# Kernel optimization log

Hardware: AMD Instinct MI355X
Metric: run time of the kernel (lower is better)

## Reference

```python
import jax, jax.numpy as jnp
import numpy as np

V, E, HN, HH, D, T, B = 10000, 512, 1024, 256, 4, 128, 64


def setup_inputs() -> dict:
    key = jax.random.key(0)
    ks = jax.random.split(key, 9)
    s = lambda k, shape: jax.random.normal(k, shape, jnp.float32) * 0.02
    return {
        "x": jax.random.randint(ks[0], (B, T), 0, V),
        "embed": s(ks[1], (V, E)),
        "Whh": s(ks[2], (2 * HH, HH)), "bhh": jnp.zeros((2 * HH,), jnp.float32),
        "Wih": s(ks[3], (2 * HH, E)), "bih": jnp.zeros((2 * HH,), jnp.float32),
        "Wh": s(ks[4], (2 * HN, HN)), "bh": jnp.zeros((2 * HN,), jnp.float32),
        "Wi": s(ks[5], (2 * HN, E)), "bi": jnp.zeros((2 * HN,), jnp.float32),
        "Wup": s(ks[6], (HN, HH)), "bup": jnp.zeros((HN,), jnp.float32),
        "Wout": s(ks[7], (V, HN)), "bout": jnp.zeros((V,), jnp.float32),
    }


def _gate(Ws, s):
    # highwayGate: split into carry/transform halves (eval mode: no gate dropout)
    hh, tt = jnp.split(Ws, 2, axis=1)
    tt = jax.nn.sigmoid(tt)
    return jnp.tanh(hh) * tt + s * (1.0 - tt)


def reference(x, embed, Whh, bhh, Wih, bih, Wh, bh, Wi, bi, Wup, bup, Wout, bout):
    emb = embed[x]                      # [B, T, E]
    xs = jnp.swapaxes(emb, 0, 1)        # [T, B, E] for scan over time

    def step(carry, xt):
        sH, sN = carry
        for i in range(D):  # depth: weights SHARED across all i (ModuleList(depth*[m]))
            Ws = sH @ Whh.T + bhh
            if i == 0:
                Ws = Ws + xt @ Wih.T + bih
            sH = _gate(Ws, sH)
            z = sH @ Wup.T + bup        # [B, HN]
            zz = jnp.concatenate([z, z], axis=1)  # scale both gate halves
            Ws = (sN @ Wh.T + bh) * zz  # HyperLinear: row-scaled linear
            if i == 0:
                Ws = Ws + (xt @ Wi.T + bi) * zz
            sN = _gate(Ws, sN)
        return (sH, sN), sN

    init = (jnp.zeros((B, HH), jnp.float32), jnp.zeros((B, HN), jnp.float32))
    _, outs = jax.lax.scan(step, init, xs)   # outs: [T, B, HN]
    h = jnp.swapaxes(outs, 0, 1)             # [B, T, HN]
    return h @ Wout.T + bout                 # [B, T, V]
```

## Files before the change

### kernel.cpp

```cpp
#include <hip/hip_runtime.h>
#include <hip/hip_cooperative_groups.h>

namespace cg = cooperative_groups;

typedef float v2f __attribute__((ext_vector_type(2)));

#define B_  64
#define T_  128
#define E_  512
#define HH_ 256
#define HN_ 1024
#define D_  4
#define V_  10000
#define NR_ (T_*D_)
#define NWG_ 256

#define WH_STR   1032
#define WI_STR   520
#define WS_STR   264
#define WH_OFF   0
#define WU_OFF   8256
#define WI_OFF   9312
#define WHH_OFF  13472
#define WIH_OFF  21920
#define LDS_FLOATS 38560

__device__ __forceinline__ float row16_sum(float x) {
    int v = __builtin_bit_cast(int, x);
    x += __builtin_bit_cast(float, __builtin_amdgcn_update_dpp(0, v, 0xB1, 0xF, 0xF, true));
    v = __builtin_bit_cast(int, x);
    x += __builtin_bit_cast(float, __builtin_amdgcn_update_dpp(0, v, 0x4E, 0xF, 0xF, true));
    v = __builtin_bit_cast(int, x);
    x += __builtin_bit_cast(float, __builtin_amdgcn_update_dpp(0, v, 0x124, 0xF, 0xF, true));
    v = __builtin_bit_cast(int, x);
    x += __builtin_bit_cast(float, __builtin_amdgcn_update_dpp(0, v, 0x128, 0xF, 0xF, true));
    return x;
}

__device__ __forceinline__ float sel4(int s, float a, float b, float c, float d) {
    return s == 0 ? a : (s == 1 ? b : (s == 2 ? c : d));
}

__device__ __forceinline__ void flag_barrier(int* __restrict__ flags,
                                             int* __restrict__ gen,
                                             int w, int tau, int target)
{
    __syncthreads();
    if (tau == 0) {
        __builtin_amdgcn_fence(__ATOMIC_RELEASE, "agent");
        __hip_atomic_store(&flags[w * 16], target, __ATOMIC_RELAXED,
                           __HIP_MEMORY_SCOPE_AGENT);
    }
    if (w == 0) {
        if (tau < NWG_) {
            while (__hip_atomic_load(&flags[tau * 16], __ATOMIC_RELAXED,
                                     __HIP_MEMORY_SCOPE_AGENT) < target) {
                __builtin_amdgcn_s_sleep(1);
            }
        }
        __syncthreads();
        if (tau == 0)
            __hip_atomic_store(gen, target, __ATOMIC_RELAXED,
                               __HIP_MEMORY_SCOPE_AGENT);
    } else if (tau == 0) {
        while (__hip_atomic_load(gen, __ATOMIC_RELAXED,
                                 __HIP_MEMORY_SCOPE_AGENT) < target) {
            __builtin_amdgcn_s_sleep(1);
        }
    }
    if (tau == 0)
        __builtin_amdgcn_fence(__ATOMIC_ACQUIRE, "agent");
    __syncthreads();
}

__global__ __launch_bounds__(1024, 1) void recur_kernel(
    const int*   __restrict__ xx,
    const float* __restrict__ embed,
    const float* __restrict__ Whh, const float* __restrict__ bhh,
    const float* __restrict__ Wih, const float* __restrict__ bih,
    const float* __restrict__ Wh,  const float* __restrict__ bh,
    const float* __restrict__ Wi,  const float* __restrict__ bi,
    const float* __restrict__ Wup, const float* __restrict__ bup,
    float* __restrict__ sH,
    float* __restrict__ sN,
    float* __restrict__ hOut,
    int*   __restrict__ flags,
    int*   __restrict__ gen)
{
    extern __shared__ float lds[];
    cg::grid_group grid = cg::this_grid();
    const int w   = blockIdx.x;
    const int tau = threadIdx.x;
    const int gid = w * 1024 + tau;
    const int ch0 = (w & 15) * 16;

    for (int idx = tau; idx < 2048; idx += 1024) {
        int r = idx >> 8, kq = idx & 255;
        int grow = w*4 + (r & 3) + (r >> 2) * HN_;
        *(float4*)&lds[WH_OFF + r*WH_STR + kq*4] =
            *(const float4*)(Wh + (size_t)grow * HN_ + kq*4);
    }
    if (tau < 256) {
        int r = tau >> 6, kq = tau & 63;
        *(float4*)&lds[WU_OFF + r*WS_STR + kq*4] =
            *(const float4*)(Wup + (size_t)(w*4 + r) * HH_ + kq*4);
    }
    if (tau < 1024) {
        int r = tau >> 7, kq = tau & 127;
        int grow = w*4 + (r & 3) + (r >> 2) * HN_;
        *(float4*)&lds[WI_OFF + r*WI_STR + kq*4] =
            *(const float4*)(Wi + (size_t)grow * E_ + kq*4);
    }
    for (int idx = tau; idx < 2048; idx += 1024) {
        int r = idx >> 6, kq = idx & 63;
        int grow = ch0 + (r & 15) + (r >> 4) * HH_;
        *(float4*)&lds[WHH_OFF + r*WS_STR + kq*4] =
            *(const float4*)(Whh + (size_t)grow * HH_ + kq*4);
    }
    for (int idx = tau; idx < 4096; idx += 1024) {
        int r = idx >> 7, kq = idx & 127;
        int grow = ch0 + (r & 15) + (r >> 4) * HH_;
        *(float4*)&lds[WIH_OFF + r*WI_STR + kq*4] =
            *(const float4*)(Wih + (size_t)grow * E_ + kq*4);
    }

    if (gid < B_ * HH_) sH[gid] = 0.f;
    if (gid < B_ * HN_) sN[B_ * HN_ + gid] = 0.f;
    if (tau == 0) flags[w * 16] = 0;
    if (w == 0 && tau == 0) *gen = 0;
    __syncthreads();
    grid.sync();

    const int lane = tau & 63;
    const int bq   = tau >> 6;
    const int kk   = lane & 15;
    const int jj   = lane >> 4;

    const int j = w * 4 + jj;
    const float bh1 = bh[j],  bh2 = bh[j + HN_];
    const float bi1 = bi[j],  bi2 = bi[j + HN_];
    const float bupj = bup[j];
    const float* wrow1 = lds + WH_OFF + jj * WH_STR;
    const float* wrow2 = lds + WH_OFF + (4 + jj) * WH_STR;
    const float* urow  = lds + WU_OFF + jj * WS_STR;
    const float* yrow1 = lds + WI_OFF + jj * WI_STR;
    const float* yrow2 = lds + WI_OFF + (4 + jj) * WI_STR;

    const int ch = ch0 + bq;
    const int bH = (w >> 4) * 4 + jj;
    const float bhh1 = bhh[ch], bhh2 = bhh[ch + HH_];
    const float bih1 = bih[ch], bih2 = bih[ch + HH_];
    const float* qrow1 = lds + WHH_OFF + bq * WS_STR;
    const float* qrow2 = lds + WHH_OFF + (16 + bq) * WS_STR;
    const float* prow1 = lds + WIH_OFF + bq * WI_STR;
    const float* prow2 = lds + WIH_OFF + (16 + bq) * WI_STR;

    for (int r = 0; r <= NR_; ++r) {
        const int p = r & 1;
        const float* sNp = sN + p * (B_ * HN_);
        const float* sHp = sH + p * (B_ * HH_);
        float* sNn = sN + (1 - p) * (B_ * HN_);
        float* sHn = sH + (1 - p) * (B_ * HH_);

        if (r >= 1) {
            const int s = r - 1;
            const int t = s >> 2;
            const int i = s & 3;

            const float* sb0 = sNp + (bq * 4 + 0) * HN_;
            const float* sb1 = sNp + (bq * 4 + 1) * HN_;
            const float* sb2 = sNp + (bq * 4 + 2) * HN_;
            const float* sb3 = sNp + (bq * 4 + 3) * HN_;

            v2f A1[4], A2[4], Z[4];
            #pragma unroll
            for (int bb = 0; bb < 4; ++bb) { A1[bb] = (v2f){0.f,0.f}; A2[bb] = (v2f){0.f,0.f}; Z[bb] = (v2f){0.f,0.f}; }

            #pragma unroll
            for (int u = 0; u < 16; ++u) {
                const int fi = (u * 16 + kk) * 4;
                float4 w1 = *(const float4*)(wrow1 + fi);
                float4 w2 = *(const float4*)(wrow2 + fi);
                float4 s0 = *(const float4*)(sb0 + fi);
                float4 s1 = *(const float4*)(sb1 + fi);
                float4 s2 = *(const float4*)(sb2 + fi);
                float4 s3 = *(const float4*)(sb3 + fi);
                v2f w1l = {w1.x, w1.y}, w1h = {w1.z, w1.w};
                v2f w2l = {w2.x, w2.y}, w2h = {w2.z, w2.w};
                v2f a;
                a = (v2f){s0.x, s0.y}; A1[0] += a * w1l; A2[0] += a * w2l;
                a = (v2f){s0.z, s0.w}; A1[0] += a * w1h; A2[0] += a * w2h;
                a = (v2f){s1.x, s1.y}; A1[1] += a * w1l; A2[1] += a * w2l;
                a = (v2f){s1.z, s1.w}; A1[1] += a * w1h; A2[1] += a * w2h;
                a = (v2f){s2.x, s2.y}; A1[2] += a * w1l; A2[2] += a * w2l;
                a = (v2f){s2.z, s2.w}; A1[2] += a * w1h; A2[2] += a * w2h;
                a = (v2f){s3.x, s3.y}; A1[3] += a * w1l; A2[3] += a * w2l;
                a = (v2f){s3.z, s3.w}; A1[3] += a * w1h; A2[3] += a * w2h;
            }

            if (i == 0) {
                const int t0 = xx[(bq * 4 + 0) * T_ + t];
                const int t1 = xx[(bq * 4 + 1) * T_ + t];
                const int t2 = xx[(bq * 4 + 2) * T_ + t];
                const int t3 = xx[(bq * 4 + 3) * T_ + t];
                const float* e0 = embed + (size_t)t0 * E_;
                const float* e1 = embed + (size_t)t1 * E_;
                const float* e2 = embed + (size_t)t2 * E_;
                const float* e3 = embed + (size_t)t3 * E_;
                #pragma unroll
                for (int u = 0; u < 8; ++u) {
                    const int fi = (u * 16 + kk) * 4;
                    float4 y1 = *(const float4*)(yrow1 + fi);
                    float4 y2 = *(const float4*)(yrow2 + fi);
                    float4 v0 = *(const float4*)(e0 + fi);
                    float4 v1 = *(const float4*)(e1 + fi);
                    float4 v2 = *(const float4*)(e2 + fi);
                    float4 v3 = *(const float4*)(e3 + fi);
                    v2f y1l = {y1.x, y1.y}, y1h = {y1.z, y1.w};
                    v2f y2l = {y2.x, y2.y}, y2h = {y2.z, y2.w};
                    v2f a;
                    a = (v2f){v0.x, v0.y}; A1[0] += a * y1l; A2[0] += a * y2l;
                    a = (v2f){v0.z, v0.w}; A1[0] += a * y1h; A2[0] += a * y2h;
                    a = (v2f){v1.x, v1.y}; A1[1] += a * y1l; A2[1] += a * y2l;
                    a = (v2f){v1.z, v1.w}; A1[1] += a * y1h; A2[1] += a * y2h;
                    a = (v2f){v2.x, v2.y}; A1[2] += a * y1l; A2[2] += a * y2l;
                    a = (v2f){v2.z, v2.w}; A1[2] += a * y1h; A2[2] += a * y2h;
                    a = (v2f){v3.x, v3.y}; A1[3] += a * y1l; A2[3] += a * y2l;
                    a = (v2f){v3.z, v3.w}; A1[3] += a * y1h; A2[3] += a * y2h;
                }
            }

            {
                const float* hb0 = sHp + (bq * 4 + 0) * HH_;
                const float* hb1 = sHp + (bq * 4 + 1) * HH_;
                const float* hb2 = sHp + (bq * 4 + 2) * HH_;
                const float* hb3 = sHp + (bq * 4 + 3) * HH_;
                #pragma unroll
                for (int u = 0; u < 4; ++u) {
                    const int fi = (u * 16 + kk) * 4;
                    float4 uw = *(const float4*)(urow + fi);
                    float4 h0 = *(const float4*)(hb0 + fi);
                    float4 h1 = *(const float4*)(hb1 + fi);
                    float4 h2 = *(const float4*)(hb2 + fi);
                    float4 h3 = *(const float4*)(hb3 + fi);
                    v2f ul = {uw.x, uw.y}, uh = {uw.z, uw.w};
                    v2f a;
                    a = (v2f){h0.x, h0.y}; Z[0] += a * ul;
                    a = (v2f){h0.z, h0.w}; Z[0] += a * uh;
                    a = (v2f){h1.x, h1.y}; Z[1] += a * ul;
                    a = (v2f){h1.z, h1.w}; Z[1] += a * uh;
                    a = (v2f){h2.x, h2.y}; Z[2] += a * ul;
                    a = (v2f){h2.z, h2.w}; Z[2] += a * uh;
                    a = (v2f){h3.x, h3.y}; Z[3] += a * ul;
                    a = (v2f){h3.z, h3.w}; Z[3] += a * uh;
                }
            }

            float a1r0 = row16_sum(A1[0].x + A1[0].y);
            float a1r1 = row16_sum(A1[1].x + A1[1].y);
            float a1r2 = row16_sum(A1[2].x + A1[2].y);
            float a1r3 = row16_sum(A1[3].x + A1[3].y);
            float a2r0 = row16_sum(A2[0].x + A2[0].y);
            float a2r1 = row16_sum(A2[1].x + A2[1].y);
            float a2r2 = row16_sum(A2[2].x + A2[2].y);
            float a2r3 = row16_sum(A2[3].x + A2[3].y);
            float zr0  = row16_sum(Z[0].x + Z[0].y);
            float zr1  = row16_sum(Z[1].x + Z[1].y);
            float zr2  = row16_sum(Z[2].x + Z[2].y);
            float zr3  = row16_sum(Z[3].x + Z[3].y);

            const int bsel = bq * 4 + (kk & 3);
            const float ov = sNp[bsel * HN_ + j];

            if (kk < 4) {
                float g1 = sel4(kk, a1r0, a1r1, a1r2, a1r3) + bh1;
                float g2 = sel4(kk, a2r0, a2r1, a2r2, a2r3) + bh2;
                if (i == 0) { g1 += bi1; g2 += bi2; }
                const float zv  = sel4(kk, zr0, zr1, zr2, zr3) + bupj;
                const float g_h = g1 * zv;
                const float g_t = g2 * zv;
                const float sg  = 1.f / (1.f + expf(-g_t));
                const float nv  = tanhf(g_h) * sg + ov * (1.f - sg);
                sNn[bsel * HN_ + j] = nv;
                if (i == D_ - 1) hOut[(size_t)(bsel * T_ + t) * HN_ + j] = nv;
            }
        }

        if (r < NR_) {
            const int t = r >> 2;
            const int i = r & 3;
            v2f a1v = {0.f, 0.f}, a2v = {0.f, 0.f};
            const float* shb = sHp + bH * HH_;
            #pragma unroll
            for (int uu = 0; uu < 4; ++uu) {
                const int fi = (((jj + uu) & 3) * 16 + kk) * 4;
                float4 q1 = *(const float4*)(qrow1 + fi);
                float4 q2 = *(const float4*)(qrow2 + fi);
                float4 sv = *(const float4*)(shb + fi);
                v2f q1l = {q1.x, q1.y}, q1h = {q1.z, q1.w};
                v2f q2l = {q2.x, q2.y}, q2h = {q2.z, q2.w};
                v2f a;
                a = (v2f){sv.x, sv.y}; a1v += a * q1l; a2v += a * q2l;
                a = (v2f){sv.z, sv.w}; a1v += a * q1h; a2v += a * q2h;
            }
            if (i == 0) {
                const int tok = xx[bH * T_ + t];
                const float* eb = embed + (size_t)tok * E_;
                #pragma unroll
                for (int uu = 0; uu < 4; ++uu) {
                    const int fi = (((jj + uu) & 3) * 16 + kk) * 4;
                    float4 p1a = *(const float4*)(prow1 + fi);
                    float4 p1b = *(const float4*)(prow1 + fi + 256);
                    float4 p2a = *(const float4*)(prow2 + fi);
                    float4 p2b = *(const float4*)(prow2 + fi + 256);
                    float4 ea  = *(const float4*)(eb + fi);
                    float4 eb2 = *(const float4*)(eb + fi + 256);
                    v2f a;
                    a = (v2f){ea.x, ea.y};  a1v += a * (v2f){p1a.x, p1a.y}; a2v += a * (v2f){p2a.x, p2a.y};
                    a = (v2f){ea.z, ea.w};  a1v += a * (v2f){p1a.z, p1a.w}; a2v += a * (v2f){p2a.z, p2a.w};
                    a = (v2f){eb2.x, eb2.y}; a1v += a * (v2f){p1b.x, p1b.y}; a2v += a * (v2f){p2b.x, p2b.y};
                    a = (v2f){eb2.z, eb2.w}; a1v += a * (v2f){p1b.z, p1b.w}; a2v += a * (v2f){p2b.z, p2b.w};
                }
            }
            float a1 = row16_sum(a1v.x + a1v.y);
            float a2 = row16_sum(a2v.x + a2v.y);
            const float ovh = sHp[bH * HH_ + ch];
            if (kk == 0) {
                a1 += bhh1; a2 += bhh2;
                if (i == 0) { a1 += bih1; a2 += bih2; }
                const float sg = 1.f / (1.f + expf(-a2));
                sHn[bH * HH_ + ch] = tanhf(a1) * sg + ovh * (1.f - sg);
            }
        }

        flag_barrier(flags, gen, w, tau, r + 1);
    }
}

__global__ __launch_bounds__(256) void out_gemm(
    const float* __restrict__ hb, const float* __restrict__ Wout,
    const float* __restrict__ bout, float* __restrict__ op)
{
    __shared__ float Ht[32][64];
    __shared__ float Wt[32][64];
    const int tau = threadIdx.x;
    const int tx  = tau & 15;
    const int ty  = tau >> 4;
    const int m0  = blockIdx.x * 64;
    const int n0  = blockIdx.y * 64;
    float acc[4][4] = {{0.f}};

    for (int k0 = 0; k0 < HN_; k0 += 32) {
        #pragma unroll
        for (int l = 0; l < 2; ++l) {
            const int f   = tau + l * 256;
            const int row = f >> 3;
            const int kq  = (f & 7) * 4;
            float4 hv = *(const float4*)(hb + (size_t)(m0 + row) * HN_ + k0 + kq);
            Ht[kq + 0][row] = hv.x; Ht[kq + 1][row] = hv.y;
            Ht[kq + 2][row] = hv.z; Ht[kq + 3][row] = hv.w;
            const int vr = n0 + row;
            float4 wv = (vr < V_) ? *(const float4*)(Wout + (size_t)vr * HN_ + k0 + kq)
                                  : make_float4(0.f, 0.f, 0.f, 0.f);
            Wt[kq + 0][row] = wv.x; Wt[kq + 1][row] = wv.y;
            Wt[kq + 2][row] = wv.z; Wt[kq + 3][row] = wv.w;
        }
        __syncthreads();
        #pragma unroll
        for (int kq = 0; kq < 32; ++kq) {
            float4 av = *(const float4*)(&Ht[kq][ty * 4]);
            float4 bv = *(const float4*)(&Wt[kq][tx * 4]);
            acc[0][0] += av.x * bv.x; acc[0][1] += av.x * bv.y;
            acc[0][2] += av.x * bv.z; acc[0][3] += av.x * bv.w;
            acc[1][0] += av.y * bv.x; acc[1][1] += av.y * bv.y;
            acc[1][2] += av.y * bv.z; acc[1][3] += av.y * bv.w;
            acc[2][0] += av.z * bv.x; acc[2][1] += av.z * bv.y;
            acc[2][2] += av.z * bv.z; acc[2][3] += av.z * bv.w;
            acc[3][0] += av.w * bv.x; acc[3][1] += av.w * bv.y;
            acc[3][2] += av.w * bv.z; acc[3][3] += av.w * bv.w;
        }
        __syncthreads();
    }

    #pragma unroll
    for (int ii = 0; ii < 4; ++ii) {
        const int m = m0 + ty * 4 + ii;
        #pragma unroll
        for (int jq = 0; jq < 4; ++jq) {
            const int v = n0 + tx * 4 + jq;
            if (v < V_) op[(size_t)m * V_ + v] = acc[ii][jq] + bout[v];
        }
    }
}

extern "C" void kernel_launch(void* const* d_in, const int* in_sizes, int n_in,
                              void* d_out, int out_size, void* d_ws, size_t ws_size,
                              hipStream_t stream) {
    const int*   xx    = (const int*)  d_in[0];
    const float* embed = (const float*)d_in[1];
    const float* Whh   = (const float*)d_in[2];
    const float* bhh   = (const float*)d_in[3];
    const float* Wih   = (const float*)d_in[4];
    const float* bih   = (const float*)d_in[5];
    const float* Wh    = (const float*)d_in[6];
    const float* bh    = (const float*)d_in[7];
    const float* Wi    = (const float*)d_in[8];
    const float* bi    = (const float*)d_in[9];
    const float* Wup   = (const float*)d_in[10];
    const float* bup   = (const float*)d_in[11];
    const float* Wout  = (const float*)d_in[12];
    const float* bout  = (const float*)d_in[13];

    float* ws   = (float*)d_ws;
    float* hbuf = ws;
    float* sHb  = hbuf + (size_t)B_ * T_ * HN_;
    float* sNb  = sHb + 2 * B_ * HH_;
    int*   flg  = (int*)(sNb + 2 * B_ * HN_);
    int*   gen  = flg + NWG_ * 16;

    void* args[] = { (void*)&xx, (void*)&embed, (void*)&Whh, (void*)&bhh,
                     (void*)&Wih, (void*)&bih, (void*)&Wh, (void*)&bh,
                     (void*)&Wi, (void*)&bi, (void*)&Wup, (void*)&bup,
                     (void*)&sHb, (void*)&sNb, (void*)&hbuf,
                     (void*)&flg, (void*)&gen };
    hipLaunchCooperativeKernel(reinterpret_cast<void*>(recur_kernel),
                               dim3(256), dim3(1024), args,
                               (size_t)(LDS_FLOATS * 4), stream);

    out_gemm<<<dim3(T_ * B_ / 64, (V_ + 63) / 64), 256, 0, stream>>>(
        hbuf, Wout, bout, (float*)d_out);
}
```

Before: 13.29 ms.

## Replace agent-scope fences with device-coherent atomic loads/stores for recurrent state

Reads and writes of the shared recurrent state (sH, sN) now go through relaxed agent-scope atomic loads and stores, which bypass non-coherent caching. This lets the grid barrier drop the heavyweight agent release and acquire fences, replacing them with a vmcnt wait and a workgroup-scope acquire. Separately, the output GEMM's LDS tiles are padded from 64 to 68 columns to reduce bank conflicts. The risk is that the split 8-byte atomic loads are slower than 16-byte vector loads, and that the weaker fences may not order every global access correctly.

```diff
diff --git a/kernel.cpp b/kernel.cpp
--- a/kernel.cpp
+++ b/kernel.cpp
@@ -24,6 +24,26 @@
 #define WHH_OFF  13472
 #define WIH_OFF  21920
 #define LDS_FLOATS 38560
+
+__device__ __forceinline__ v2f ld2_dev(const float* p) {
+    unsigned long long a = __hip_atomic_load((const unsigned long long*)p,
+                                             __ATOMIC_RELAXED, __HIP_MEMORY_SCOPE_AGENT);
+    return __builtin_bit_cast(v2f, a);
+}
+__device__ __forceinline__ float4 ld4_dev(const float* p) {
+    v2f lo = ld2_dev(p);
+    v2f hi = ld2_dev(p + 2);
+    return make_float4(lo.x, lo.y, hi.x, hi.y);
+}
+__device__ __forceinline__ float ld1_dev(const float* p) {
+    unsigned v = __hip_atomic_load((const unsigned*)p,
+                                   __ATOMIC_RELAXED, __HIP_MEMORY_SCOPE_AGENT);
+    return __builtin_bit_cast(float, v);
+}
+__device__ __forceinline__ void st1_dev(float* p, float v) {
+    __hip_atomic_store((unsigned*)p, __builtin_bit_cast(unsigned, v),
+                       __ATOMIC_RELAXED, __HIP_MEMORY_SCOPE_AGENT);
+}
 
 __device__ __forceinline__ float row16_sum(float x) {
     int v = __builtin_bit_cast(int, x);
@@ -47,7 +67,7 @@
 {
     __syncthreads();
     if (tau == 0) {
-        __builtin_amdgcn_fence(__ATOMIC_RELEASE, "agent");
+        asm volatile("s_waitcnt vmcnt(0)" ::: "memory");
         __hip_atomic_store(&flags[w * 16], target, __ATOMIC_RELAXED,
                            __HIP_MEMORY_SCOPE_AGENT);
     }
@@ -68,8 +88,7 @@
             __builtin_amdgcn_s_sleep(1);
         }
     }
-    if (tau == 0)
-        __builtin_amdgcn_fence(__ATOMIC_ACQUIRE, "agent");
+    __builtin_amdgcn_fence(__ATOMIC_ACQUIRE, "workgroup");
     __syncthreads();
 }
 
@@ -181,10 +200,10 @@
                 const int fi = (u * 16 + kk) * 4;
                 float4 w1 = *(const float4*)(wrow1 + fi);
                 float4 w2 = *(const float4*)(wrow2 + fi);
-                float4 s0 = *(const float4*)(sb0 + fi);
-                float4 s1 = *(const float4*)(sb1 + fi);
-                float4 s2 = *(const float4*)(sb2 + fi);
-                float4 s3 = *(const float4*)(sb3 + fi);
+                float4 s0 = ld4_dev(sb0 + fi);
+                float4 s1 = ld4_dev(sb1 + fi);
+                float4 s2 = ld4_dev(sb2 + fi);
+                float4 s3 = ld4_dev(sb3 + fi);
                 v2f w1l = {w1.x, w1.y}, w1h = {w1.z, w1.w};
                 v2f w2l = {w2.x, w2.y}, w2h = {w2.z, w2.w};
                 v2f a;
@@ -239,10 +258,10 @@
                 for (int u = 0; u < 4; ++u) {
                     const int fi = (u * 16 + kk) * 4;
                     float4 uw = *(const float4*)(urow + fi);
-                    float4 h0 = *(const float4*)(hb0 + fi);
-                    float4 h1 = *(const float4*)(hb1 + fi);
-                    float4 h2 = *(const float4*)(hb2 + fi);
-                    float4 h3 = *(const float4*)(hb3 + fi);
+                    float4 h0 = ld4_dev(hb0 + fi);
+                    float4 h1 = ld4_dev(hb1 + fi);
+                    float4 h2 = ld4_dev(hb2 + fi);
+                    float4 h3 = ld4_dev(hb3 + fi);
                     v2f ul = {uw.x, uw.y}, uh = {uw.z, uw.w};
                     v2f a;
                     a = (v2f){h0.x, h0.y}; Z[0] += a * ul;
@@ -270,7 +289,7 @@
             float zr3  = row16_sum(Z[3].x + Z[3].y);
 
             const int bsel = bq * 4 + (kk & 3);
-            const float ov = sNp[bsel * HN_ + j];
+            const float ov = ld1_dev(sNp + bsel * HN_ + j);
 
             if (kk < 4) {
                 float g1 = sel4(kk, a1r0, a1r1, a1r2, a1r3) + bh1;
@@ -281,7 +300,7 @@
                 const float g_t = g2 * zv;
                 const float sg  = 1.f / (1.f + expf(-g_t));
                 const float nv  = tanhf(g_h) * sg + ov * (1.f - sg);
-                sNn[bsel * HN_ + j] = nv;
+                st1_dev(sNn + bsel * HN_ + j, nv);
                 if (i == D_ - 1) hOut[(size_t)(bsel * T_ + t) * HN_ + j] = nv;
             }
         }
@@ -296,7 +315,7 @@
                 const int fi = (((jj + uu) & 3) * 16 + kk) * 4;
                 float4 q1 = *(const float4*)(qrow1 + fi);
                 float4 q2 = *(const float4*)(qrow2 + fi);
-                float4 sv = *(const float4*)(shb + fi);
+                float4 sv = ld4_dev(shb + fi);
                 v2f q1l = {q1.x, q1.y}, q1h = {q1.z, q1.w};
                 v2f q2l = {q2.x, q2.y}, q2h = {q2.z, q2.w};
                 v2f a;
@@ -324,12 +343,12 @@
             }
             float a1 = row16_sum(a1v.x + a1v.y);
             float a2 = row16_sum(a2v.x + a2v.y);
-            const float ovh = sHp[bH * HH_ + ch];
+            const float ovh = ld1_dev(sHp + bH * HH_ + ch);
             if (kk == 0) {
                 a1 += bhh1; a2 += bhh2;
                 if (i == 0) { a1 += bih1; a2 += bih2; }
                 const float sg = 1.f / (1.f + expf(-a2));
-                sHn[bH * HH_ + ch] = tanhf(a1) * sg + ovh * (1.f - sg);
+                st1_dev(sHn + bH * HH_ + ch, tanhf(a1) * sg + ovh * (1.f - sg));
             }
         }
 
@@ -341,8 +360,8 @@
     const float* __restrict__ hb, const float* __restrict__ Wout,
     const float* __restrict__ bout, float* __restrict__ op)
 {
-    __shared__ float Ht[32][64];
-    __shared__ float Wt[32][64];
+    __shared__ float Ht[32][68];
+    __shared__ float Wt[32][68];
     const int tau = threadIdx.x;
     const int tx  = tau & 15;
     const int ty  = tau >> 4;
```

New measurement: 15.10 ms. 13.6% more time.

## Hold Wup/Whh slices in registers and enlarge output GEMM tiles to 128x128

Applied to the files above, without the earlier changes.

The recurrent kernel now loads each thread's Wup and Whh weight slices into registers once, instead of keeping them in LDS and re-reading them every step. This shrinks the LDS footprint and cuts LDS traffic per step, at the cost of extra VGPRs in a 1024-thread block. Separately, the output projection GEMM moves from 64x64 tiles with 4x4 per-thread accumulators to 128x128 tiles with 8x8 accumulators and a K-step of 16. This raises arithmetic intensity per LDS load, but uses more registers and launches fewer blocks.

```diff
diff --git a/kernel.cpp b/kernel.cpp
--- a/kernel.cpp
+++ b/kernel.cpp
@@ -17,13 +17,10 @@
 
 #define WH_STR   1032
 #define WI_STR   520
-#define WS_STR   264
 #define WH_OFF   0
-#define WU_OFF   8256
-#define WI_OFF   9312
-#define WHH_OFF  13472
-#define WIH_OFF  21920
-#define LDS_FLOATS 38560
+#define WI_OFF   8256
+#define WIH_OFF  12416
+#define LDS_FLOATS 29056
 
 __device__ __forceinline__ float row16_sum(float x) {
     int v = __builtin_bit_cast(int, x);
@@ -100,22 +97,11 @@
         *(float4*)&lds[WH_OFF + r*WH_STR + kq*4] =
             *(const float4*)(Wh + (size_t)grow * HN_ + kq*4);
     }
-    if (tau < 256) {
-        int r = tau >> 6, kq = tau & 63;
-        *(float4*)&lds[WU_OFF + r*WS_STR + kq*4] =
-            *(const float4*)(Wup + (size_t)(w*4 + r) * HH_ + kq*4);
-    }
     if (tau < 1024) {
         int r = tau >> 7, kq = tau & 127;
         int grow = w*4 + (r & 3) + (r >> 2) * HN_;
         *(float4*)&lds[WI_OFF + r*WI_STR + kq*4] =
             *(const float4*)(Wi + (size_t)grow * E_ + kq*4);
-    }
-    for (int idx = tau; idx < 2048; idx += 1024) {
-        int r = idx >> 6, kq = idx & 63;
-        int grow = ch0 + (r & 15) + (r >> 4) * HH_;
-        *(float4*)&lds[WHH_OFF + r*WS_STR + kq*4] =
-            *(const float4*)(Whh + (size_t)grow * HH_ + kq*4);
     }
     for (int idx = tau; idx < 4096; idx += 1024) {
         int r = idx >> 7, kq = idx & 127;
@@ -142,16 +128,23 @@
     const float bupj = bup[j];
     const float* wrow1 = lds + WH_OFF + jj * WH_STR;
     const float* wrow2 = lds + WH_OFF + (4 + jj) * WH_STR;
-    const float* urow  = lds + WU_OFF + jj * WS_STR;
     const float* yrow1 = lds + WI_OFF + jj * WI_STR;
     const float* yrow2 = lds + WI_OFF + (4 + jj) * WI_STR;
+    float4 ureg[4];
+    #pragma unroll
+    for (int u = 0; u < 4; ++u)
+        ureg[u] = *(const float4*)(Wup + (size_t)j * HH_ + (u*16 + kk)*4);
 
     const int ch = ch0 + bq;
     const int bH = (w >> 4) * 4 + jj;
     const float bhh1 = bhh[ch], bhh2 = bhh[ch + HH_];
     const float bih1 = bih[ch], bih2 = bih[ch + HH_];
-    const float* qrow1 = lds + WHH_OFF + bq * WS_STR;
-    const float* qrow2 = lds + WHH_OFF + (16 + bq) * WS_STR;
+    float4 qreg1[4], qreg2[4];
+    #pragma unroll
+    for (int c = 0; c < 4; ++c) {
+        qreg1[c] = *(const float4*)(Whh + (size_t)ch * HH_ + (c*16 + kk)*4);
+        qreg2[c] = *(const float4*)(Whh + (size_t)(ch + HH_) * HH_ + (c*16 + kk)*4);
+    }
     const float* prow1 = lds + WIH_OFF + bq * WI_STR;
     const float* prow2 = lds + WIH_OFF + (16 + bq) * WI_STR;
 
@@ -238,7 +231,7 @@
                 #pragma unroll
                 for (int u = 0; u < 4; ++u) {
                     const int fi = (u * 16 + kk) * 4;
-                    float4 uw = *(const float4*)(urow + fi);
+                    float4 uw = ureg[u];
                     float4 h0 = *(const float4*)(hb0 + fi);
                     float4 h1 = *(const float4*)(hb1 + fi);
                     float4 h2 = *(const float4*)(hb2 + fi);
@@ -292,10 +285,10 @@
             v2f a1v = {0.f, 0.f}, a2v = {0.f, 0.f};
             const float* shb = sHp + bH * HH_;
             #pragma unroll
-            for (int uu = 0; uu < 4; ++uu) {
-                const int fi = (((jj + uu) & 3) * 16 + kk) * 4;
-                float4 q1 = *(const float4*)(qrow1 + fi);
-                float4 q2 = *(const float4*)(qrow2 + fi);
+            for (int c = 0; c < 4; ++c) {
+                const int fi = (c * 16 + kk) * 4;
+                float4 q1 = qreg1[c];
+                float4 q2 = qreg2[c];
                 float4 sv = *(const float4*)(shb + fi);
                 v2f q1l = {q1.x, q1.y}, q1h = {q1.z, q1.w};
                 v2f q2l = {q2.x, q2.y}, q2h = {q2.z, q2.w};
@@ -341,21 +334,21 @@
     const float* __restrict__ hb, const float* __restrict__ Wout,
     const float* __restrict__ bout, float* __restrict__ op)
 {
-    __shared__ float Ht[32][64];
-    __shared__ float Wt[32][64];
+    __shared__ float Ht[16][132];
+    __shared__ float Wt[16][132];
     const int tau = threadIdx.x;
     const int tx  = tau & 15;
     const int ty  = tau >> 4;
-    const int m0  = blockIdx.x * 64;
-    const int n0  = blockIdx.y * 64;
-    float acc[4][4] = {{0.f}};
-
-    for (int k0 = 0; k0 < HN_; k0 += 32) {
+    const int m0  = blockIdx.x * 128;
+    const int n0  = blockIdx.y * 128;
+    float acc[8][8] = {{0.f}};
+
+    for (int k0 = 0; k0 < HN_; k0 += 16) {
         #pragma unroll
         for (int l = 0; l < 2; ++l) {
-            const int f   = tau + l * 256;
-            const int row = f >> 3;
-            const int kq  = (f & 7) * 4;
+            const int idx = l * 256 + tau;
+            const int row = idx >> 2;
+            const int kq  = (idx & 3) * 4;
             float4 hv = *(const float4*)(hb + (size_t)(m0 + row) * HN_ + k0 + kq);
             Ht[kq + 0][row] = hv.x; Ht[kq + 1][row] = hv.y;
             Ht[kq + 2][row] = hv.z; Ht[kq + 3][row] = hv.w;
@@ -367,27 +360,28 @@
         }
         __syncthreads();
         #pragma unroll
-        for (int kq = 0; kq < 32; ++kq) {
-            float4 av = *(const float4*)(&Ht[kq][ty * 4]);
-            float4 bv = *(const float4*)(&Wt[kq][tx * 4]);
-            acc[0][0] += av.x * bv.x; acc[0][1] += av.x * bv.y;
-            acc[0][2] += av.x * bv.z; acc[0][3] += av.x * bv.w;
-            acc[1][0] += av.y * bv.x; acc[1][1] += av.y * bv.y;
-            acc[1][2] += av.y * bv.z; acc[1][3] += av.y * bv.w;
-            acc[2][0] += av.z * bv.x; acc[2][1] += av.z * bv.y;
-            acc[2][2] += av.z * bv.z; acc[2][3] += av.z * bv.w;
-            acc[3][0] += av.w * bv.x; acc[3][1] += av.w * bv.y;
-            acc[3][2] += av.w * bv.z; acc[3][3] += av.w * bv.w;
+        for (int k = 0; k < 16; ++k) {
+            float4 a0 = *(const float4*)(&Ht[k][ty * 8]);
+            float4 a1 = *(const float4*)(&Ht[k][ty * 8 + 4]);
+            float4 b0 = *(const float4*)(&Wt[k][tx * 8]);
+            float4 b1 = *(const float4*)(&Wt[k][tx * 8 + 4]);
+            const float am[8] = {a0.x,a0.y,a0.z,a0.w,a1.x,a1.y,a1.z,a1.w};
+            const float bn[8] = {b0.x,b0.y,b0.z,b0.w,b1.x,b1.y,b1.z,b1.w};
+            #pragma unroll
+            for (int ii = 0; ii < 8; ++ii)
+                #pragma unroll
+                for (int jq = 0; jq < 8; ++jq)
+                    acc[ii][jq] += am[ii] * bn[jq];
         }
         __syncthreads();
     }
 
     #pragma unroll
-    for (int ii = 0; ii < 4; ++ii) {
-        const int m = m0 + ty * 4 + ii;
+    for (int ii = 0; ii < 8; ++ii) {
+        const int m = m0 + ty * 8 + ii;
         #pragma unroll
-        for (int jq = 0; jq < 4; ++jq) {
-            const int v = n0 + tx * 4 + jq;
+        for (int jq = 0; jq < 8; ++jq) {
+            const int v = n0 + tx * 8 + jq;
             if (v < V_) op[(size_t)m * V_ + v] = acc[ii][jq] + bout[v];
         }
     }
@@ -427,6 +421,6 @@
                                dim3(256), dim3(1024), args,
                                (size_t)(LDS_FLOATS * 4), stream);
 
-    out_gemm<<<dim3(T_ * B_ / 64, (V_ + 63) / 64), 256, 0, stream>>>(
+    out_gemm<<<dim3(T_ * B_ / 128, (V_ + 127) / 128), 256, 0, stream>>>(
         hbuf, Wout, bout, (float*)d_out);
 }
```

Measured after the change: 15.66 ms. 17.8% more time.
